# Optimization experiments

Hardware: AMD Instinct MI355X
Metric: run time of the kernel (lower is better)

Reference implementation:

```python
import jax, jax.numpy as jnp
import numpy as np

DIM = 1024          # n_embd
NUM_EXPERTS = 8
TOP_K = 2
HIDDEN = 4 * DIM // TOP_K   # expert_hidden_dim = 2048
BS, SLEN = 1, 2048


def setup_inputs() -> dict:
    key = jax.random.key(0)
    k0, k1, k2, k3 = jax.random.split(key, 4)
    x = jax.random.normal(k0, (BS, SLEN, DIM), dtype=jnp.float32)
    gate_w = jax.random.normal(k1, (NUM_EXPERTS, DIM), dtype=jnp.float32) * 0.02
    w_up = jax.random.normal(k2, (NUM_EXPERTS, HIDDEN, DIM), dtype=jnp.float32) * 0.02
    w_down = jax.random.normal(k3, (NUM_EXPERTS, DIM, HIDDEN), dtype=jnp.float32) * 0.02
    expert_bias = jnp.zeros((NUM_EXPERTS,), dtype=jnp.float32)
    return {"x": x, "gate_w": gate_w, "w_up": w_up, "w_down": w_down,
            "expert_bias": expert_bias}


def _moe(x, gate_w, w_up, w_down, expert_bias):
    bs, slen, dim = x.shape
    xf = x.reshape(-1, dim)                       # (T, D)
    # Sigmoid router (scores in fp32, bias only affects selection, not weights)
    scores = jax.nn.sigmoid(xf @ gate_w.T)        # (T, E)
    biased = scores + expert_bias
    _, sel = jax.lax.top_k(biased, TOP_K)         # (T, K) expert ids, distinct per token
    top_scores = jnp.take_along_axis(scores, sel, axis=-1)  # (T, K)

    # Scatter/gather dispatch + grouped GEMM is mathematically equivalent to:
    #   out[t] = sum_k W_down[e_tk] @ relu(W_up[e_tk] @ (s_tk * x[t]))^2
    # Loop over the small fixed expert set via lax.scan; unassigned tokens
    # contribute exactly zero (relu(0)^2 = 0), honoring the routing sparsity.
    def body(acc, ew):
        e, wu, wd = ew
        # combined routing weight for this expert per token (at most one slot)
        w_t = jnp.sum(jnp.where(sel == e, top_scores, 0.0), axis=-1)  # (T,)
        xe = xf * w_t[:, None]                    # (T, D), zero for non-routed
        h = jnp.square(jax.nn.relu(xe @ wu.T))    # (T, H)  relu(x)^2 activation
        return acc + h @ wd.T, None

    out0 = jnp.zeros_like(xf)
    out, _ = jax.lax.scan(body, out0, (jnp.arange(NUM_EXPERTS), w_up, w_down))
    return out.reshape(bs, slen, dim)


def reference(x, gate_w, w_up, w_down, expert_bias):
    return _moe(x, gate_w, w_up, w_down, expert_bias)
```

## Files before the change

### kernel.cpp

```cpp
#include <hip/hip_runtime.h>
#include <cstdint>
#include <cstddef>

#define T_TOK 2048
#define DMODEL 1024
#define NEXP 8
#define HID 2048
#define DUMP_ID 4096

typedef __bf16 bf16x8 __attribute__((ext_vector_type(8)));
typedef float f32x4 __attribute__((ext_vector_type(4)));
typedef unsigned short u16;
typedef u16 u16x8 __attribute__((ext_vector_type(8)));

__device__ __forceinline__ u16 f2bf(float f) {
    union { float f; unsigned int u; } v; v.f = f;
    unsigned int u = v.u;
    unsigned int r = (u + 0x7FFFu + ((u >> 16) & 1u)) >> 16;
    return (u16)r;
}

__device__ __forceinline__ void gl2lds16(const void* g, void* l) {
    __builtin_amdgcn_global_load_lds(
        (const __attribute__((address_space(1))) void*)g,
        (__attribute__((address_space(3))) void*)l,
        16, 0, 0);
}

__global__ __launch_bounds__(256) void fused_pre(
    const float4* __restrict__ x4, const float4* __restrict__ gw4,
    const float* __restrict__ bias, ushort4* __restrict__ xb4,
    unsigned int* __restrict__ selpack, float* __restrict__ w2,
    unsigned int* __restrict__ xb_dump_row_u32) {
    const int b = blockIdx.x;
    const int tid = threadIdx.x;

    if (b == 256) {
        if (tid < DMODEL / 2) xb_dump_row_u32[tid] = 0;
        return;
    }
    const int wv = tid >> 6;
    const int lane = tid & 63;
    const int pair = b * 4 + wv;
    const int t0 = 2 * pair, t1 = t0 + 1;

    float acc0[NEXP], acc1[NEXP];
#pragma unroll
    for (int e = 0; e < NEXP; ++e) { acc0[e] = 0.f; acc1[e] = 0.f; }
#pragma unroll
    for (int j = 0; j < 4; ++j) {
        int i4 = lane + j * 64;
        float4 a0 = x4[t0 * 256 + i4];
        float4 a1 = x4[t1 * 256 + i4];
        ushort4 s0, s1;
        s0.x = f2bf(a0.x); s0.y = f2bf(a0.y); s0.z = f2bf(a0.z); s0.w = f2bf(a0.w);
        s1.x = f2bf(a1.x); s1.y = f2bf(a1.y); s1.z = f2bf(a1.z); s1.w = f2bf(a1.w);
        xb4[t0 * 256 + i4] = s0;
        xb4[t1 * 256 + i4] = s1;
#pragma unroll
        for (int e = 0; e < NEXP; ++e) {
            float4 g = gw4[e * 256 + i4];
            acc0[e] += a0.x * g.x + a0.y * g.y + a0.z * g.z + a0.w * g.w;
            acc1[e] += a1.x * g.x + a1.y * g.y + a1.z * g.z + a1.w * g.w;
        }
    }
#pragma unroll
    for (int e = 0; e < NEXP; ++e)
        for (int off = 32; off > 0; off >>= 1) {
            acc0[e] += __shfl_xor(acc0[e], off, 64);
            acc1[e] += __shfl_xor(acc1[e], off, 64);
        }
    if (lane == 0) {
#pragma unroll
        for (int tt = 0; tt < 2; ++tt) {
            int t = tt ? t1 : t0;
            float sc[NEXP], bi[NEXP];
#pragma unroll
            for (int e = 0; e < NEXP; ++e) {
                float a = tt ? acc1[e] : acc0[e];
                sc[e] = 1.f / (1.f + expf(-a));
                bi[e] = sc[e] + bias[e];
            }
            int e0 = 0;
            for (int e = 1; e < NEXP; ++e) if (bi[e] > bi[e0]) e0 = e;
            int e1 = -1;
            for (int e = 0; e < NEXP; ++e) {
                if (e == e0) continue;
                if (e1 < 0 || bi[e] > bi[e1]) e1 = e;
            }
            selpack[t] = (unsigned int)e0 | ((unsigned int)e1 << 8);
            w2[2 * t]     = sc[e0] * sc[e0];
            w2[2 * t + 1] = sc[e1] * sc[e1];
        }
    }
}

__global__ __launch_bounds__(256) void build_lists(
    const unsigned int* __restrict__ selpack, int* __restrict__ counts,
    int* __restrict__ list) {
    const int e = blockIdx.x;
    const int tid = threadIdx.x;
    const int lane = tid & 63;
    const int wv = tid >> 6;
    __shared__ int wsum[4];
    __shared__ int base;
    if (tid == 0) base = 0;
    __syncthreads();
    for (int tb = 0; tb < T_TOK; tb += 256) {
        int t = tb + tid;
        unsigned int sp = selpack[t];
        bool f1 = ((sp >> 8) & 255u) == (unsigned)e;
        bool f = ((sp & 255u) == (unsigned)e) | f1;
        int id = 2 * t + (f1 ? 1 : 0);
        unsigned long long m = __ballot(f);
        int pos = __popcll(m & ((1ull << lane) - 1ull));
        if (lane == 0) wsum[wv] = __popcll(m);
        __syncthreads();
        int woff = 0;
#pragma unroll
        for (int i = 0; i < 4; ++i) if (i < wv) woff += wsum[i];
        int bse = base;
        if (f) list[e * T_TOK + bse + woff + pos] = id;
        __syncthreads();
        if (tid == 0) base = bse + wsum[0] + wsum[1] + wsum[2] + wsum[3];
    }
    __syncthreads();
    int total = base;
    if (tid == 0) counts[e] = total;
    for (int i = total + tid; i < T_TOK; i += 256) list[e * T_TOK + i] = DUMP_ID;
}

template <int MODE>
__global__ __launch_bounds__(256, 2) void moe_gemm(
    const u16* __restrict__ Asrc, const int* __restrict__ list,
    const int* __restrict__ counts, const float* __restrict__ Ball32,
    const float* __restrict__ w2, u16* __restrict__ Hout,
    float* __restrict__ Cout) {
    constexpr int K   = (MODE == 0) ? DMODEL : HID;
    constexpr int N   = (MODE == 0) ? HID : DMODEL;
    constexpr int NKT = K / 64;
    constexpr int NTN = N / 128;
    constexpr int LOGNTN = (MODE == 0) ? 4 : 3;
    constexpr int KSP = (MODE == 0) ? 1 : 2;
    constexpr int KTPER = NKT / KSP;

    const int b = blockIdx.x;
    const int e = b & 7;
    const int rest = b >> 3;
    const int n0 = (rest & (NTN - 1)) * 128;
    const int rest2 = rest >> LOGNTN;
    const int m0 = (rest2 & 15) * 128;
    const int ks = rest2 >> 4;
    if (m0 >= counts[e]) return;
    const int kt0 = ks * KTPER, kt1 = kt0 + KTPER;

    const int tid = threadIdx.x;
    const int lane = tid & 63;
    const int w = tid >> 6;

    __shared__ u16 As[2][128 * 64];
    __shared__ u16 Bs[2][128 * 64];

    const int* mylist = list + e * T_TOK + m0;
    const float* B32 = Ball32 + (size_t)e * HID * DMODEL;

    const u16* ap[4];
    const float4* bp[4];
    int bwr[4];
    const int c8 = tid & 7;
#pragma unroll
    for (int it = 0; it < 4; ++it) {
        int row = it * 32 + (tid >> 3);
        int gs = c8 ^ (row & 7);
        int id = mylist[row];
        int arow = (MODE == 0) ? (id >> 1) : id;
        ap[it] = Asrc + (size_t)arow * K + gs * 8;
        bp[it] = (const float4*)(B32 + (size_t)(n0 + row) * K) + c8 * 2;
        bwr[it] = row * 64 + gs * 8;
    }

    const int wm = (w >> 1) * 64;
    const int wn = (w & 1) * 64;
    const int quad = lane >> 4;
    const int lrow = lane & 15;

    f32x4 acc[4][4];
#pragma unroll
    for (int i = 0; i < 4; ++i)
#pragma unroll
        for (int j = 0; j < 4; ++j) acc[i][j] = f32x4{0.f, 0.f, 0.f, 0.f};

    float4 bu[4][2];

    auto stageA = [&](int kt, int buf) {
#pragma unroll
        for (int it = 0; it < 4; ++it)
            gl2lds16(ap[it] + kt * 64, &As[buf][(it * 256 + w * 64) * 8]);
    };
    auto loadB = [&](int kt) {
#pragma unroll
        for (int it = 0; it < 4; ++it) {
            bu[it][0] = bp[it][kt * 16];
            bu[it][1] = bp[it][kt * 16 + 1];
        }
    };
    auto writeB = [&](int buf) {
#pragma unroll
        for (int it = 0; it < 4; ++it) {
            u16x8 o;
            o[0] = f2bf(bu[it][0].x); o[1] = f2bf(bu[it][0].y);
            o[2] = f2bf(bu[it][0].z); o[3] = f2bf(bu[it][0].w);
            o[4] = f2bf(bu[it][1].x); o[5] = f2bf(bu[it][1].y);
            o[6] = f2bf(bu[it][1].z); o[7] = f2bf(bu[it][1].w);
            *(u16x8*)&Bs[buf][bwr[it]] = o;
        }
    };
    auto compute = [&](int buf) {
#pragma unroll
        for (int s = 0; s < 2; ++s) {
            const int q = s * 4 + quad;
            bf16x8 af[4], bfr[4];
#pragma unroll
            for (int i = 0; i < 4; ++i) {
                int ra = wm + i * 16 + lrow;
                int rb = wn + i * 16 + lrow;
                af[i]  = *(const bf16x8*)&As[buf][ra * 64 + (q ^ (ra & 7)) * 8];
                bfr[i] = *(const bf16x8*)&Bs[buf][rb * 64 + (q ^ (rb & 7)) * 8];
            }
#pragma unroll
            for (int i = 0; i < 4; ++i)
#pragma unroll
                for (int j = 0; j < 4; ++j)
                    acc[i][j] = __builtin_amdgcn_mfma_f32_16x16x32_bf16(
                        af[i], bfr[j], acc[i][j], 0, 0, 0);
        }
    };

    stageA(kt0, 0);
    loadB(kt0);
    writeB(0);
    __syncthreads();

    for (int kt = kt0; kt < kt1; ++kt) {
        const int cur = (kt - kt0) & 1;
        const int nxt = cur ^ 1;
        const bool more = (kt + 1 < kt1);
        if (more) {
            stageA(kt + 1, nxt);
            loadB(kt + 1);
        }
        compute(cur);
        if (more) writeB(nxt);
        __syncthreads();
    }

#pragma unroll
    for (int i = 0; i < 4; ++i) {
        int mbase = wm + i * 16 + (lane >> 4) * 4;
        int ids[4];
        float ww[4];
#pragma unroll
        for (int r = 0; r < 4; ++r) {
            ids[r] = mylist[mbase + r];
            if (MODE == 0) ww[r] = w2[ids[r]];
        }
#pragma unroll
        for (int j = 0; j < 4; ++j) {
            int n = n0 + wn + j * 16 + (lane & 15);
#pragma unroll
            for (int r = 0; r < 4; ++r) {
                float v = acc[i][j][r];
                if (MODE == 0) {
                    v = (v > 0.f) ? v * v * ww[r] : 0.f;
                    Hout[(size_t)ids[r] * HID + n] = f2bf(v);
                } else {
                    if (ids[r] != DUMP_ID)
                        atomicAdd(&Cout[(size_t)(ids[r] >> 1) * DMODEL + n], v);
                }
            }
        }
    }
}

extern "C" void kernel_launch(void* const* d_in, const int* in_sizes, int n_in,
                              void* d_out, int out_size, void* d_ws, size_t ws_size,
                              hipStream_t stream) {
    const float* x      = (const float*)d_in[0];
    const float* gate_w = (const float*)d_in[1];
    const float* w_up   = (const float*)d_in[2];
    const float* w_down = (const float*)d_in[3];
    const float* bias   = (const float*)d_in[4];
    float* out = (float*)d_out;

    char* p = (char*)d_ws;
    int* counts = (int*)p;                 p += 256;
    int* list   = (int*)p;                 p += NEXP * T_TOK * 4;
    float* w2   = (float*)p;               p += 4104 * 4;
    unsigned int* selpack = (unsigned int*)p;  p += T_TOK * 4;
    u16* xb  = (u16*)p;  p += (size_t)(T_TOK + 1) * DMODEL * 2;
    u16* h   = (u16*)p;  p += (size_t)(2 * T_TOK + 1) * HID * 2;

    hipMemsetAsync(d_out, 0, (size_t)out_size * sizeof(float), stream);

    fused_pre<<<257, 256, 0, stream>>>(
        (const float4*)x, (const float4*)gate_w, bias,
        (ushort4*)xb, selpack, w2,
        (unsigned int*)(xb + (size_t)T_TOK * DMODEL));

    build_lists<<<NEXP, 256, 0, stream>>>(selpack, counts, list);

    moe_gemm<0><<<16 * (HID / 128) * NEXP, 256, 0, stream>>>(
        xb, list, counts, w_up, w2, h, nullptr);

    moe_gemm<1><<<2 * 16 * (DMODEL / 128) * NEXP, 256, 0, stream>>>(
        h, list, counts, w_down, w2, nullptr, out);
}
```

Measured before the change: 271.2 us.

## Enlarge MoE GEMM M-tile to 256 with 512-thread blocks and XCD-aware mapping

Both expert GEMMs now use 512-thread workgroups computing 256x128 output tiles instead of 128x128. Each fp32 weight tile loaded and converted to bf16 is reused across twice as many token rows, which halves the redundant weight traffic and conversion work. Block indices are remapped so consecutive blocks on the same XCD share an expert. The B tile is now single-buffered in LDS to make room for the larger A buffer, which adds an extra barrier per k-step and loses some load/compute overlap. Partly filled experts also waste more work per tile because of the coarser M granularity.

```diff
diff --git a/kernel.cpp b/kernel.cpp
--- a/kernel.cpp
+++ b/kernel.cpp
@@ -131,7 +131,7 @@
 }
 
 template <int MODE>
-__global__ __launch_bounds__(256, 2) void moe_gemm(
+__global__ __launch_bounds__(512, 2) void moe_gemm(
     const u16* __restrict__ Asrc, const int* __restrict__ list,
     const int* __restrict__ counts, const float* __restrict__ Ball32,
     const float* __restrict__ w2, u16* __restrict__ Hout,
@@ -144,13 +144,13 @@
     constexpr int KSP = (MODE == 0) ? 1 : 2;
     constexpr int KTPER = NKT / KSP;
 
-    const int b = blockIdx.x;
-    const int e = b & 7;
-    const int rest = b >> 3;
-    const int n0 = (rest & (NTN - 1)) * 128;
-    const int rest2 = rest >> LOGNTN;
-    const int m0 = (rest2 & 15) * 128;
-    const int ks = rest2 >> 4;
+    const int wg = ((int)blockIdx.x & 7) * ((int)gridDim.x >> 3) + ((int)blockIdx.x >> 3);
+    const int e  = wg >> 7;
+    const int r  = wg & 127;
+    const int n0 = (r & (NTN - 1)) * 128;
+    const int mi = (r >> LOGNTN) & 7;
+    const int ks = r >> (LOGNTN + 3);
+    const int m0 = mi * 256;
     if (m0 >= counts[e]) return;
     const int kt0 = ks * KTPER, kt1 = kt0 + KTPER;
 
@@ -158,23 +158,28 @@
     const int lane = tid & 63;
     const int w = tid >> 6;
 
-    __shared__ u16 As[2][128 * 64];
-    __shared__ u16 Bs[2][128 * 64];
+    __shared__ u16 As[2][256 * 64];
+    __shared__ u16 Bs[128 * 64];
 
     const int* mylist = list + e * T_TOK + m0;
     const float* B32 = Ball32 + (size_t)e * HID * DMODEL;
 
     const u16* ap[4];
-    const float4* bp[4];
-    int bwr[4];
+    const float4* bp[2];
+    int bwr[2];
     const int c8 = tid & 7;
 #pragma unroll
     for (int it = 0; it < 4; ++it) {
-        int row = it * 32 + (tid >> 3);
+        int row = it * 64 + (tid >> 3);
         int gs = c8 ^ (row & 7);
         int id = mylist[row];
         int arow = (MODE == 0) ? (id >> 1) : id;
         ap[it] = Asrc + (size_t)arow * K + gs * 8;
+    }
+#pragma unroll
+    for (int it = 0; it < 2; ++it) {
+        int row = it * 64 + (tid >> 3);
+        int gs = c8 ^ (row & 7);
         bp[it] = (const float4*)(B32 + (size_t)(n0 + row) * K) + c8 * 2;
         bwr[it] = row * 64 + gs * 8;
     }
@@ -190,29 +195,29 @@
 #pragma unroll
         for (int j = 0; j < 4; ++j) acc[i][j] = f32x4{0.f, 0.f, 0.f, 0.f};
 
-    float4 bu[4][2];
+    float4 bu[2][2];
 
     auto stageA = [&](int kt, int buf) {
 #pragma unroll
         for (int it = 0; it < 4; ++it)
-            gl2lds16(ap[it] + kt * 64, &As[buf][(it * 256 + w * 64) * 8]);
+            gl2lds16(ap[it] + kt * 64, &As[buf][(it * 64 + w * 8) * 64]);
     };
     auto loadB = [&](int kt) {
 #pragma unroll
-        for (int it = 0; it < 4; ++it) {
+        for (int it = 0; it < 2; ++it) {
             bu[it][0] = bp[it][kt * 16];
             bu[it][1] = bp[it][kt * 16 + 1];
         }
     };
-    auto writeB = [&](int buf) {
-#pragma unroll
-        for (int it = 0; it < 4; ++it) {
+    auto writeB = [&]() {
+#pragma unroll
+        for (int it = 0; it < 2; ++it) {
             u16x8 o;
             o[0] = f2bf(bu[it][0].x); o[1] = f2bf(bu[it][0].y);
             o[2] = f2bf(bu[it][0].z); o[3] = f2bf(bu[it][0].w);
             o[4] = f2bf(bu[it][1].x); o[5] = f2bf(bu[it][1].y);
             o[6] = f2bf(bu[it][1].z); o[7] = f2bf(bu[it][1].w);
-            *(u16x8*)&Bs[buf][bwr[it]] = o;
+            *(u16x8*)&Bs[bwr[it]] = o;
         }
     };
     auto compute = [&](int buf) {
@@ -225,7 +230,7 @@
                 int ra = wm + i * 16 + lrow;
                 int rb = wn + i * 16 + lrow;
                 af[i]  = *(const bf16x8*)&As[buf][ra * 64 + (q ^ (ra & 7)) * 8];
-                bfr[i] = *(const bf16x8*)&Bs[buf][rb * 64 + (q ^ (rb & 7)) * 8];
+                bfr[i] = *(const bf16x8*)&Bs[rb * 64 + (q ^ (rb & 7)) * 8];
             }
 #pragma unroll
             for (int i = 0; i < 4; ++i)
@@ -236,22 +241,25 @@
         }
     };
 
+    loadB(kt0);
     stageA(kt0, 0);
-    loadB(kt0);
-    writeB(0);
+    writeB();
     __syncthreads();
 
+    int cur = 0;
     for (int kt = kt0; kt < kt1; ++kt) {
-        const int cur = (kt - kt0) & 1;
-        const int nxt = cur ^ 1;
         const bool more = (kt + 1 < kt1);
         if (more) {
-            stageA(kt + 1, nxt);
             loadB(kt + 1);
+            stageA(kt + 1, cur ^ 1);
         }
         compute(cur);
-        if (more) writeB(nxt);
         __syncthreads();
+        if (more) {
+            writeB();
+            __syncthreads();
+            cur ^= 1;
+        }
     }
 
 #pragma unroll
@@ -260,22 +268,22 @@
         int ids[4];
         float ww[4];
 #pragma unroll
-        for (int r = 0; r < 4; ++r) {
-            ids[r] = mylist[mbase + r];
-            if (MODE == 0) ww[r] = w2[ids[r]];
+        for (int rr = 0; rr < 4; ++rr) {
+            ids[rr] = mylist[mbase + rr];
+            if (MODE == 0) ww[rr] = w2[ids[rr]];
         }
 #pragma unroll
         for (int j = 0; j < 4; ++j) {
             int n = n0 + wn + j * 16 + (lane & 15);
 #pragma unroll
-            for (int r = 0; r < 4; ++r) {
-                float v = acc[i][j][r];
+            for (int rr = 0; rr < 4; ++rr) {
+                float v = acc[i][j][rr];
                 if (MODE == 0) {
-                    v = (v > 0.f) ? v * v * ww[r] : 0.f;
-                    Hout[(size_t)ids[r] * HID + n] = f2bf(v);
+                    v = (v > 0.f) ? v * v * ww[rr] : 0.f;
+                    Hout[(size_t)ids[rr] * HID + n] = f2bf(v);
                 } else {
-                    if (ids[r] != DUMP_ID)
-                        atomicAdd(&Cout[(size_t)(ids[r] >> 1) * DMODEL + n], v);
+                    if (ids[rr] != DUMP_ID)
+                        atomicAdd(&Cout[(size_t)(ids[rr] >> 1) * DMODEL + n], v);
                 }
             }
         }
@@ -309,9 +317,9 @@
 
     build_lists<<<NEXP, 256, 0, stream>>>(selpack, counts, list);
 
-    moe_gemm<0><<<16 * (HID / 128) * NEXP, 256, 0, stream>>>(
+    moe_gemm<0><<<NEXP * 128, 512, 0, stream>>>(
         xb, list, counts, w_up, w2, h, nullptr);
 
-    moe_gemm<1><<<2 * 16 * (DMODEL / 128) * NEXP, 256, 0, stream>>>(
+    moe_gemm<1><<<NEXP * 128, 512, 0, stream>>>(
         h, list, counts, w_down, w2, nullptr, out);
 }
```

Measured after the change: 258.4 us. 4.7% less time.
